# Performance work log

Hardware: AMD Instinct MI355X
Metric: run time of the kernel (lower is better)

The kernel has to match this reference:

```python
import jax, jax.numpy as jnp
import numpy as np


def setup_inputs() -> dict:
    key = jax.random.key(0)
    ks = jax.random.split(key, 7)
    b, c, h, w = 4, 256, 64, 64
    ci = c // 2
    inp = {
        "x0": jax.random.normal(ks[0], (b, 2 * c, h, w), dtype=jnp.float32),
        "x": jax.random.normal(ks[1], (b, c, h, w), dtype=jnp.float32),
        "x_dsm": jax.random.normal(ks[2], (b, c, h, w), dtype=jnp.float32),
        # 1x1 conv weights, stored as [out_ch, in_ch]
        "w_phi": jax.random.normal(ks[3], (ci, c), dtype=jnp.float32) * 0.02,
        "w_theta": jax.random.normal(ks[4], (ci, c), dtype=jnp.float32) * 0.02,
        "w_g": jax.random.normal(ks[5], (c, 2 * c), dtype=jnp.float32) * 0.02,
        "w_mask": jax.random.normal(ks[6], (2 * c, c), dtype=jnp.float32) * 0.02,
    }
    return inp


def reference(x0, x, x_dsm, w_phi, w_theta, w_g, w_mask):
    b, c, h, w = x.shape
    ci = c // 2
    n = h * w
    # 1x1 convs as channel matmuls
    phi = jnp.einsum('oc,bchw->bohw', w_phi, x).reshape(b, ci, n)            # [b, ci, N]
    theta = jnp.einsum('oc,bchw->bohw', w_theta, x_dsm).reshape(b, ci, n)    # [b, ci, N]
    theta = theta.transpose(0, 2, 1)                                         # [b, N, ci]
    g = jnp.einsum('oc,bchw->bohw', w_g, x0).reshape(b, c, n).transpose(0, 2, 1)  # [b, N, c]
    scores = jnp.matmul(theta, phi)                                          # [b, N, N]
    # NOTE: original uses nn.Softmax(dim=1) -> normalize over the FIRST N axis
    attn = jax.nn.softmax(scores, axis=1)
    out = jnp.matmul(attn, g)                                                # [b, N, c]
    out = out.transpose(0, 2, 1).reshape(b, c, h, w)
    mask = jnp.einsum('oc,bchw->bohw', w_mask, out)                          # [b, 2c, h, w]
    return mask + x0
```

## Files before the change

### kernel.cpp

```cpp
#include <hip/hip_runtime.h>
#include <math.h>

#define NB 4
#define NC 256
#define NCI 128
#define NC2 512
#define NPOS 4096
#define ISPLIT 8

using bf16x8 = __attribute__((ext_vector_type(8))) short;
using f32x4  = __attribute__((ext_vector_type(4))) float;

__device__ inline unsigned short f2bf(float f) {
  unsigned int u = __float_as_uint(f);
  u = (u + 0x7fffu + ((u >> 16) & 1u)) >> 16;
  return (unsigned short)u;
}
__device__ inline float bf2f(short s) {
  return __uint_as_float(((unsigned int)(unsigned short)s) << 16);
}

__global__ void k_cast4(const float* __restrict__ s0, short* __restrict__ d0, int n0,
                        const float* __restrict__ s1, short* __restrict__ d1, int n1,
                        const float* __restrict__ s2, short* __restrict__ d2, int n2,
                        const float* __restrict__ s3, short* __restrict__ d3, int n3) {
  int i = blockIdx.x * 256 + threadIdx.x;
  if (i < n0) { d0[i] = (short)f2bf(s0[i]); return; } i -= n0;
  if (i < n1) { d1[i] = (short)f2bf(s1[i]); return; } i -= n1;
  if (i < n2) { d2[i] = (short)f2bf(s2[i]); return; } i -= n2;
  if (i < n3) { d3[i] = (short)f2bf(s3[i]); }
}

__global__ __launch_bounds__(256) void k_tcast_all(
    const float* __restrict__ x, const float* __restrict__ xdsm,
    const float* __restrict__ x0, short* __restrict__ xT,
    short* __restrict__ xdT, short* __restrict__ x0T) {
  __shared__ float t[64][65];
  const int tid = threadIdx.x;
  const int y = blockIdx.y, c0 = blockIdx.x * 64, b = blockIdx.z;
  const float* in; short* out; int R, r0;
  if (y < 4)      { in = x;    out = xT;  R = NC;  r0 = y * 64; }
  else if (y < 8) { in = xdsm; out = xdT; R = NC;  r0 = (y - 4) * 64; }
  else            { in = x0;   out = x0T; R = NC2; r0 = (y - 8) * 64; }
  const size_t inBs = (size_t)R * NPOS, outBs = (size_t)NPOS * R;
  {
    int r = tid >> 2, cc = (tid & 3) * 16;
    const float* ib = in + (size_t)b * inBs + (size_t)(r0 + r) * NPOS + c0 + cc;
#pragma unroll
    for (int i = 0; i < 4; ++i) {
      float4 v = *(const float4*)(ib + i * 4);
      t[r][cc + i * 4 + 0] = v.x; t[r][cc + i * 4 + 1] = v.y;
      t[r][cc + i * 4 + 2] = v.z; t[r][cc + i * 4 + 3] = v.w;
    }
  }
  __syncthreads();
  {
    int c = tid >> 2, rr = (tid & 3) * 16;
    __align__(16) short v[16];
#pragma unroll
    for (int i = 0; i < 16; ++i) v[i] = (short)f2bf(t[rr + i][c]);
    short* ob = out + (size_t)b * outBs + (size_t)(c0 + c) * R + r0 + rr;
    *(int4*)(ob) = *(const int4*)(v);
    *(int4*)(ob + 8) = *(const int4*)(v + 8);
  }
}

__global__ __launch_bounds__(256) void k_tcast4(
    const short* __restrict__ inP, short* __restrict__ out) {
  __shared__ float t[64][65];
  const int tid = threadIdx.x;
  const int r0 = blockIdx.y * 64, c0 = blockIdx.x * 64, b = blockIdx.z;
  {
    int r = tid >> 2, cc = (tid & 3) * 16;
    float tacc[16] = {};
#pragma unroll
    for (int p = 0; p < 4; ++p) {
      const short* ib = inP + ((size_t)p * NB + b) * NC * NPOS +
                        (size_t)(r0 + r) * NPOS + c0 + cc;
      bf16x8 a = *(const bf16x8*)(ib);
      bf16x8 a2 = *(const bf16x8*)(ib + 8);
#pragma unroll
      for (int i = 0; i < 8; ++i) { tacc[i] += bf2f(a[i]); tacc[8 + i] += bf2f(a2[i]); }
    }
#pragma unroll
    for (int i = 0; i < 16; ++i) t[r][cc + i] = tacc[i];
  }
  __syncthreads();
  {
    int c = tid >> 2, rr = (tid & 3) * 16;
    __align__(16) short v[16];
#pragma unroll
    for (int i = 0; i < 16; ++i) v[i] = (short)f2bf(t[rr + i][c]);
    short* ob = out + (size_t)b * (size_t)NPOS * NC + (size_t)(c0 + c) * NC + r0 + rr;
    *(int4*)(ob) = *(const int4*)(v);
    *(int4*)(ob + 8) = *(const int4*)(v + 8);
  }
}

template<bool OUT_BF16, bool HAS_RES>
__global__ __launch_bounds__(256, 2) void k_gemm(
    const short* __restrict__ A, const short* __restrict__ B,
    void* __restrict__ outv, const float* __restrict__ res,
    int K, int sN, size_t aBs, size_t bBs, size_t oBs) {
  __shared__ short As[2][64 * 64];
  __shared__ short Bs_[2][64 * 64];
  const int tid = threadIdx.x, lane = tid & 63, w = tid >> 6;
  const int x = lane & 15, q = lane >> 4;
  const int wm = (w & 1) * 32, wn = (w >> 1) * 32;
  const int n0 = blockIdx.x * 64, m0 = blockIdx.y * 64, b = blockIdx.z;
  const short* Ab = A + (size_t)b * aBs + (size_t)m0 * K;
  const short* Bb = B + (size_t)b * bBs + (size_t)n0 * K;
  const int r = tid >> 2, cth = tid & 3;
  f32x4 acc[2][2];
  acc[0][0] = acc[0][1] = acc[1][0] = acc[1][1] = (f32x4){0.f, 0.f, 0.f, 0.f};
  int4 ra[2], rb[2];
  const int NK = K >> 6;
#define GLOAD(kt)                                                              \
  { _Pragma("unroll") for (int i = 0; i < 2; ++i) {                            \
      ra[i] = *(const int4*)(Ab + (size_t)r * K + (kt) * 64 + (cth + i * 4) * 8); \
      rb[i] = *(const int4*)(Bb + (size_t)r * K + (kt) * 64 + (cth + i * 4) * 8); } }
#define GWRITE(buf)                                                            \
  { _Pragma("unroll") for (int i = 0; i < 2; ++i) {                            \
      *(int4*)(&As[buf][r * 64 + (((cth + i * 4) ^ (r & 7)) * 8)]) = ra[i];    \
      *(int4*)(&Bs_[buf][r * 64 + (((cth + i * 4) ^ (r & 7)) * 8)]) = rb[i]; } }
  GLOAD(0); GWRITE(0); __syncthreads();
  int cur = 0;
  for (int kt = 0; kt < NK; ++kt) {
    if (kt + 1 < NK) GLOAD(kt + 1);
    bf16x8 af[2][2], bfr[2][2];
#pragma unroll
    for (int ms = 0; ms < 2; ++ms) {
      int rowm = wm + ms * 16 + x;
#pragma unroll
      for (int ks = 0; ks < 2; ++ks)
        af[ms][ks] = *(const bf16x8*)(&As[cur][rowm * 64 + (((ks * 4 + q) ^ (rowm & 7)) * 8)]);
    }
#pragma unroll
    for (int ns = 0; ns < 2; ++ns) {
      int rown = wn + ns * 16 + x;
#pragma unroll
      for (int ks = 0; ks < 2; ++ks)
        bfr[ns][ks] = *(const bf16x8*)(&Bs_[cur][rown * 64 + (((ks * 4 + q) ^ (rown & 7)) * 8)]);
    }
#pragma unroll
    for (int ms = 0; ms < 2; ++ms)
#pragma unroll
      for (int ns = 0; ns < 2; ++ns)
#pragma unroll
        for (int ks = 0; ks < 2; ++ks)
          acc[ms][ns] = __builtin_amdgcn_mfma_f32_16x16x32_bf16(
              af[ms][ks], bfr[ns][ks], acc[ms][ns], 0, 0, 0);
    if (kt + 1 < NK) GWRITE(cur ^ 1);
    __syncthreads();
    cur ^= 1;
  }
#pragma unroll
  for (int ms = 0; ms < 2; ++ms)
#pragma unroll
    for (int ns = 0; ns < 2; ++ns) {
      int n = n0 + wn + ns * 16 + x;
      int m = m0 + wm + ms * 16 + q * 4;
      size_t off = (size_t)b * oBs + (size_t)n * sN + m;
      if (OUT_BF16) {
        __align__(8) short pv[4];
#pragma unroll
        for (int j = 0; j < 4; ++j) pv[j] = (short)f2bf(acc[ms][ns][j]);
        *(uint2*)((short*)outv + off) = *(const uint2*)pv;
      } else {
        float4 v = {acc[ms][ns][0], acc[ms][ns][1], acc[ms][ns][2], acc[ms][ns][3]};
        if (HAS_RES) {
          float4 rv = *(const float4*)(res + off);
          v.x += rv.x; v.y += rv.y; v.z += rv.z; v.w += rv.w;
        }
        *(float4*)((float*)outv + off) = v;
      }
    }
#undef GLOAD
#undef GWRITE
}

__global__ __launch_bounds__(256, 4) void k_lsum(
    const short* __restrict__ phiB, const short* __restrict__ thetaB,
    float* __restrict__ plsum) {
  __shared__ short thT[2][64 * 128];
  const int tid = threadIdx.x, lane = tid & 63, w = tid >> 6;
  const int x = lane & 15, q = lane >> 4;
  const int j0 = blockIdx.x * 64, iy = blockIdx.y, b = blockIdx.z;
  const short* phb = phiB + (size_t)b * NPOS * NCI;
  const short* thb = thetaB + (size_t)b * NPOS * NCI + (size_t)iy * (NPOS / ISPLIT) * NCI;
  bf16x8 af[4];
  {
    const short* pr = phb + (size_t)(j0 + w * 16 + x) * NCI;
#pragma unroll
    for (int kk = 0; kk < 4; ++kk) af[kk] = *(const bf16x8*)(pr + kk * 32 + q * 8);
  }
  float lsum[4] = {0.f, 0.f, 0.f, 0.f};
  int4 rt[4];
  const int NIT = NPOS / ISPLIT / 64;
#define LSUM_LOAD(it)                                                         \
  { _Pragma("unroll") for (int r = 0; r < 4; ++r) {                           \
      int s = tid + r * 256; int row = s >> 4, c = s & 15;                    \
      rt[r] = *(const int4*)(thb + (size_t)((it) * 64 + row) * NCI + c * 8); } }
#define LSUM_WRITE(buf)                                                       \
  { _Pragma("unroll") for (int r = 0; r < 4; ++r) {                           \
      int s = tid + r * 256; int row = s >> 4, c = s & 15;                    \
      *(int4*)(&thT[buf][row * 128 + ((c ^ (row & 7)) * 8)]) = rt[r]; } }
  LSUM_LOAD(0); LSUM_WRITE(0); __syncthreads();
  int cur = 0;
  for (int it = 0; it < NIT; ++it) {
    if (it + 1 < NIT) LSUM_LOAD(it + 1);
#pragma unroll
    for (int ii = 0; ii < 4; ++ii) {
      f32x4 s = {0.f, 0.f, 0.f, 0.f};
      int row = ii * 16 + x;
      int sw = row & 7;
#pragma unroll
      for (int kk = 0; kk < 4; ++kk) {
        bf16x8 bfv = *(const bf16x8*)(&thT[cur][row * 128 + (((kk * 4 + q) ^ sw) * 8)]);
        s = __builtin_amdgcn_mfma_f32_16x16x32_bf16(af[kk], bfv, s, 0, 0, 0);
      }
#pragma unroll
      for (int r = 0; r < 4; ++r) lsum[r] += __expf(s[r]);
    }
    if (it + 1 < NIT) LSUM_WRITE(cur ^ 1);
    __syncthreads();
    cur ^= 1;
  }
#pragma unroll
  for (int m = 1; m < 16; m <<= 1)
#pragma unroll
    for (int r = 0; r < 4; ++r) lsum[r] += __shfl_xor(lsum[r], m);
  if (x == 0) {
#pragma unroll
    for (int r = 0; r < 4; ++r)
      plsum[((size_t)(b * ISPLIT + iy) << 12) + j0 + w * 16 + 4 * q + r] = lsum[r];
  }
#undef LSUM_LOAD
#undef LSUM_WRITE
}

__global__ void k_lcomb(const float* __restrict__ plsum, float* __restrict__ linv) {
  int i = blockIdx.x * 256 + threadIdx.x;
  int b = i >> 12, j = i & (NPOS - 1);
  float s = 0.f;
#pragma unroll
  for (int t = 0; t < ISPLIT; ++t) s += plsum[((size_t)(b * ISPLIT + t) << 12) + j];
  linv[i] = 1.0f / s;
}

__global__ void k_scale_g(short* __restrict__ gB, const float* __restrict__ linv) {
  size_t e = ((size_t)blockIdx.x * 256 + threadIdx.x) * 8;
  int b = (int)(e >> 20);
  int p = (int)(e & (NPOS - 1));
  __align__(16) short v[8];
  *(int4*)v = *(const int4*)(gB + e);
  const float* lv = linv + ((size_t)b << 12) + p;
#pragma unroll
  for (int k = 0; k < 8; ++k) v[k] = (short)f2bf(bf2f(v[k]) * lv[k]);
  *(int4*)(gB + e) = *(const int4*)v;
}

__global__ __launch_bounds__(256, 3) void k_attn(
    const short* __restrict__ phiB, const short* __restrict__ thetaB,
    const short* __restrict__ gB, short* __restrict__ omidP) {
  __shared__ short phiT[2][32 * 128];
  __shared__ short gT[2][256 * 32];
  __shared__ short pT[4][16 * 32];
  const int tid = threadIdx.x, lane = tid & 63, w = tid >> 6;
  const int x = lane & 15, q = lane >> 4;
  const int i0 = blockIdx.x * 64, jq = blockIdx.y, b = blockIdx.z;
  const short* phb = phiB + (size_t)b * NPOS * NCI;
  const short* thb = thetaB + (size_t)b * NPOS * NCI;
  const short* gb = gB + (size_t)b * NC * NPOS;
  short* om = omidP + ((size_t)(jq * NB + b)) * NC * NPOS;

  bf16x8 tf[4];
  {
    const short* tr = thb + (size_t)(i0 + w * 16 + x) * NCI;
#pragma unroll
    for (int kk = 0; kk < 4; ++kk) tf[kk] = *(const bf16x8*)(tr + kk * 32 + q * 8);
  }
  f32x4 acc[16];
#pragma unroll
  for (int i = 0; i < 16; ++i) acc[i] = (f32x4){0.f, 0.f, 0.f, 0.f};

  const int sgx = (x & 3) ^ ((x >> 2) & 1);
  int4 rphi[2], rg[4];
  const int NT = 32;
  const int jbase = jq * 32;
#define ATTN_LOAD(jt)                                                          \
  { _Pragma("unroll") for (int r = 0; r < 2; ++r) {                            \
      int s = tid + r * 256; int row = s >> 4, c = s & 15;                     \
      rphi[r] = *(const int4*)(phb + (size_t)((jbase + (jt)) * 32 + row) * NCI + c * 8); } \
    _Pragma("unroll") for (int r = 0; r < 4; ++r) {                            \
      int s = tid + r * 256; int cc = s >> 2, c4 = s & 3;                      \
      rg[r] = *(const int4*)(gb + (size_t)cc * NPOS + (jbase + (jt)) * 32 + c4 * 8); } }
#define ATTN_WRITE(buf)                                                        \
  { _Pragma("unroll") for (int r = 0; r < 2; ++r) {                            \
      int s = tid + r * 256; int row = s >> 4, c = s & 15;                     \
      *(int4*)(&phiT[buf][row * 128 + ((c ^ (row & 7)) * 8)]) = rphi[r]; }     \
    _Pragma("unroll") for (int r = 0; r < 4; ++r) {                            \
      int s = tid + r * 256; int cc = s >> 2, c4 = s & 3;                      \
      int sw = (cc & 3) ^ ((cc >> 2) & 1);                                     \
      *(int4*)(&gT[buf][cc * 32 + ((c4 ^ sw) * 8)]) = rg[r]; } }
  ATTN_LOAD(0); ATTN_WRITE(0); __syncthreads();
  int cur = 0;
  for (int jt = 0; jt < NT; ++jt) {
    if (jt + 1 < NT) ATTN_LOAD(jt + 1);
    {
      const short* PH = &phiT[cur][0];
      const short* GT = &gT[cur][0];
      short* PW = &pT[w][0];
#pragma unroll
      for (int jsub = 0; jsub < 2; ++jsub) {
        f32x4 s = {0.f, 0.f, 0.f, 0.f};
        int row = jsub * 16 + x;
        int sw = row & 7;
#pragma unroll
        for (int kk = 0; kk < 4; ++kk) {
          bf16x8 a = *(const bf16x8*)(PH + row * 128 + (((kk * 4 + q) ^ sw) * 8));
          s = __builtin_amdgcn_mfma_f32_16x16x32_bf16(a, tf[kk], s, 0, 0, 0);
        }
        unsigned short p0 = f2bf(__expf(s[0]));
        unsigned short p1 = f2bf(__expf(s[1]));
        unsigned short p2 = f2bf(__expf(s[2]));
        unsigned short p3 = f2bf(__expf(s[3]));
        unsigned int lo = (unsigned int)p0 | ((unsigned int)p1 << 16);
        unsigned int hi = (unsigned int)p2 | ((unsigned int)p3 << 16);
        int byteoff = (x * 64 + jsub * 32 + q * 8) ^ ((((x >> 1) & 3)) << 4);
        *(uint2*)((char*)PW + byteoff) = make_uint2(lo, hi);
      }
      {
        int c = q ^ ((x >> 1) & 3);
        bf16x8 ap = *(const bf16x8*)((const char*)PW + x * 64 + c * 16);
#pragma unroll
        for (int cf = 0; cf < 16; ++cf) {
          bf16x8 bg = *(const bf16x8*)(GT + (cf * 16 + x) * 32 + ((q ^ sgx) * 8));
          acc[cf] = __builtin_amdgcn_mfma_f32_16x16x32_bf16(ap, bg, acc[cf], 0, 0, 0);
        }
      }
    }
    if (jt + 1 < NT) ATTN_WRITE(cur ^ 1);
    __syncthreads();
    cur ^= 1;
  }
#pragma unroll
  for (int cf = 0; cf < 16; ++cf) {
    __align__(8) short pv[4];
#pragma unroll
    for (int j = 0; j < 4; ++j) pv[j] = (short)f2bf(acc[cf][j]);
    size_t o = (size_t)(cf * 16 + x) * NPOS + i0 + w * 16 + 4 * q;
    *(uint2*)(om + o) = *(const uint2*)pv;
  }
#undef ATTN_LOAD
#undef ATTN_WRITE
}

extern "C" void kernel_launch(void* const* d_in, const int* in_sizes, int n_in,
                              void* d_out, int out_size, void* d_ws, size_t ws_size,
                              hipStream_t stream) {
  (void)in_sizes; (void)n_in; (void)out_size; (void)ws_size;
  const float* x0      = (const float*)d_in[0];
  const float* x       = (const float*)d_in[1];
  const float* x_dsm   = (const float*)d_in[2];
  const float* w_phi   = (const float*)d_in[3];
  const float* w_theta = (const float*)d_in[4];
  const float* w_g     = (const float*)d_in[5];
  const float* w_mask  = (const float*)d_in[6];
  float* outp = (float*)d_out;

  short* sp = (short*)d_ws;
  short* wb_phi   = sp; sp += 32768;
  short* wb_theta = sp; sp += 32768;
  short* wb_g     = sp; sp += 131072;
  short* wb_mask  = sp; sp += 131072;
  short* xT   = sp; sp += (size_t)NB * NPOS * NC;
  short* xdT  = sp; sp += (size_t)NB * NPOS * NC;
  short* x0T  = sp; sp += (size_t)NB * NPOS * NC2;
  short* phiB   = sp; sp += (size_t)NB * NPOS * NCI;
  short* thetaB = sp; sp += (size_t)NB * NPOS * NCI;
  short* gBuf   = sp; sp += (size_t)NB * NC * NPOS;
  float* linv = (float*)sp; sp += 2 * (size_t)NB * NPOS;
  float* plsum = (float*)sp;
  short* omidP = xT;
  short* omidT = phiB;

  k_cast4<<<dim3(1280), 256, 0, stream>>>(w_phi, wb_phi, 32768,
                                          w_theta, wb_theta, 32768,
                                          w_g, wb_g, 131072,
                                          w_mask, wb_mask, 131072);

  k_tcast_all<<<dim3(64, 16, NB), 256, 0, stream>>>(x, x_dsm, x0, xT, xdT, x0T);

  k_gemm<true, false><<<dim3(64, 2, NB), 256, 0, stream>>>(
      wb_phi, xT, phiB, nullptr, NC, NCI, 0, (size_t)NPOS * NC, (size_t)NPOS * NCI);
  k_gemm<true, false><<<dim3(64, 2, NB), 256, 0, stream>>>(
      wb_theta, xdT, thetaB, nullptr, NC, NCI, 0, (size_t)NPOS * NC, (size_t)NPOS * NCI);
  k_gemm<true, false><<<dim3(4, 64, NB), 256, 0, stream>>>(
      x0T, wb_g, gBuf, nullptr, NC2, NPOS, (size_t)NPOS * NC2, 0, (size_t)NC * NPOS);

  k_lsum<<<dim3(NPOS / 64, ISPLIT, NB), 256, 0, stream>>>(phiB, thetaB, plsum);
  k_lcomb<<<dim3(NB * NPOS / 256), 256, 0, stream>>>(plsum, linv);
  k_scale_g<<<dim3(2048), 256, 0, stream>>>(gBuf, linv);

  k_attn<<<dim3(64, 4, NB), 256, 0, stream>>>(phiB, thetaB, gBuf, omidP);

  k_tcast4<<<dim3(64, 4, NB), 256, 0, stream>>>(omidP, omidT);

  k_gemm<false, true><<<dim3(8, 64, NB), 256, 0, stream>>>(
      omidT, wb_mask, outp, x0, NC, NPOS, (size_t)NPOS * NC, 0, (size_t)NC2 * NPOS);
}
```

Before: 251.9 us.

## Switch attention kernel to 32x32x16 MFMA with 128-row query tiles

```diff
diff --git a/kernel.cpp b/kernel.cpp
--- a/kernel.cpp
+++ b/kernel.cpp
@@ -10,6 +10,7 @@
 
 using bf16x8 = __attribute__((ext_vector_type(8))) short;
 using f32x4  = __attribute__((ext_vector_type(4))) float;
+using f32x16 = __attribute__((ext_vector_type(16))) float;
 
 __device__ inline unsigned short f2bf(float f) {
   unsigned int u = __float_as_uint(f);
@@ -260,31 +261,33 @@
   *(int4*)(gB + e) = *(const int4*)v;
 }
 
-__global__ __launch_bounds__(256, 3) void k_attn(
+__global__ __launch_bounds__(256, 2) void k_attn(
     const short* __restrict__ phiB, const short* __restrict__ thetaB,
     const short* __restrict__ gB, short* __restrict__ omidP) {
   __shared__ short phiT[2][32 * 128];
   __shared__ short gT[2][256 * 32];
-  __shared__ short pT[4][16 * 32];
+  __shared__ short pT[4][32 * 32];
   const int tid = threadIdx.x, lane = tid & 63, w = tid >> 6;
-  const int x = lane & 15, q = lane >> 4;
-  const int i0 = blockIdx.x * 64, jq = blockIdx.y, b = blockIdx.z;
+  const int il = lane & 31, h = lane >> 5;
+  const int key = (il >> 1) & 3;
+  const int i0 = blockIdx.x * 128, jq = blockIdx.y, b = blockIdx.z;
   const short* phb = phiB + (size_t)b * NPOS * NCI;
   const short* thb = thetaB + (size_t)b * NPOS * NCI;
   const short* gb = gB + (size_t)b * NC * NPOS;
   short* om = omidP + ((size_t)(jq * NB + b)) * NC * NPOS;
 
-  bf16x8 tf[4];
-  {
-    const short* tr = thb + (size_t)(i0 + w * 16 + x) * NCI;
-#pragma unroll
-    for (int kk = 0; kk < 4; ++kk) tf[kk] = *(const bf16x8*)(tr + kk * 32 + q * 8);
-  }
-  f32x4 acc[16];
-#pragma unroll
-  for (int i = 0; i < 16; ++i) acc[i] = (f32x4){0.f, 0.f, 0.f, 0.f};
-
-  const int sgx = (x & 3) ^ ((x >> 2) & 1);
+  bf16x8 tf[8];
+  {
+    const short* tr = thb + (size_t)(i0 + w * 32 + il) * NCI;
+#pragma unroll
+    for (int kk = 0; kk < 8; ++kk) tf[kk] = *(const bf16x8*)(tr + kk * 16 + h * 8);
+  }
+  f32x16 acc[8];
+#pragma unroll
+  for (int i = 0; i < 8; ++i)
+#pragma unroll
+    for (int r = 0; r < 16; ++r) acc[i][r] = 0.f;
+
   int4 rphi[2], rg[4];
   const int NT = 32;
   const int jbase = jq * 32;
@@ -301,42 +304,44 @@
       *(int4*)(&phiT[buf][row * 128 + ((c ^ (row & 7)) * 8)]) = rphi[r]; }     \
     _Pragma("unroll") for (int r = 0; r < 4; ++r) {                            \
       int s = tid + r * 256; int cc = s >> 2, c4 = s & 3;                      \
-      int sw = (cc & 3) ^ ((cc >> 2) & 1);                                     \
-      *(int4*)(&gT[buf][cc * 32 + ((c4 ^ sw) * 8)]) = rg[r]; } }
+      *(int4*)(&gT[buf][cc * 32 + ((c4 ^ ((cc >> 1) & 3)) * 8)]) = rg[r]; } }
   ATTN_LOAD(0); ATTN_WRITE(0); __syncthreads();
   int cur = 0;
   for (int jt = 0; jt < NT; ++jt) {
     if (jt + 1 < NT) ATTN_LOAD(jt + 1);
     {
       const short* PH = &phiT[cur][0];
+      short* PW = &pT[w][0];
+      f32x16 s16;
+#pragma unroll
+      for (int r = 0; r < 16; ++r) s16[r] = 0.f;
+      const int swp = il & 7;
+#pragma unroll
+      for (int kk = 0; kk < 8; ++kk) {
+        bf16x8 a = *(const bf16x8*)(PH + il * 128 + (((2 * kk + h) ^ swp) * 8));
+        s16 = __builtin_amdgcn_mfma_f32_32x32x16_bf16(a, tf[kk], s16, 0, 0, 0);
+      }
+#pragma unroll
+      for (int g2 = 0; g2 < 4; ++g2) {
+        unsigned short p0 = f2bf(__expf(s16[4 * g2 + 0]));
+        unsigned short p1 = f2bf(__expf(s16[4 * g2 + 1]));
+        unsigned short p2 = f2bf(__expf(s16[4 * g2 + 2]));
+        unsigned short p3 = f2bf(__expf(s16[4 * g2 + 3]));
+        unsigned int lo = (unsigned int)p0 | ((unsigned int)p1 << 16);
+        unsigned int hi2 = (unsigned int)p2 | ((unsigned int)p3 << 16);
+        *(uint2*)(PW + il * 32 + ((g2 ^ key) * 8) + 4 * h) = make_uint2(lo, hi2);
+      }
       const short* GT = &gT[cur][0];
-      short* PW = &pT[w][0];
-#pragma unroll
-      for (int jsub = 0; jsub < 2; ++jsub) {
-        f32x4 s = {0.f, 0.f, 0.f, 0.f};
-        int row = jsub * 16 + x;
-        int sw = row & 7;
-#pragma unroll
-        for (int kk = 0; kk < 4; ++kk) {
-          bf16x8 a = *(const bf16x8*)(PH + row * 128 + (((kk * 4 + q) ^ sw) * 8));
-          s = __builtin_amdgcn_mfma_f32_16x16x32_bf16(a, tf[kk], s, 0, 0, 0);
-        }
-        unsigned short p0 = f2bf(__expf(s[0]));
-        unsigned short p1 = f2bf(__expf(s[1]));
-        unsigned short p2 = f2bf(__expf(s[2]));
-        unsigned short p3 = f2bf(__expf(s[3]));
-        unsigned int lo = (unsigned int)p0 | ((unsigned int)p1 << 16);
-        unsigned int hi = (unsigned int)p2 | ((unsigned int)p3 << 16);
-        int byteoff = (x * 64 + jsub * 32 + q * 8) ^ ((((x >> 1) & 3)) << 4);
-        *(uint2*)((char*)PW + byteoff) = make_uint2(lo, hi);
-      }
-      {
-        int c = q ^ ((x >> 1) & 3);
-        bf16x8 ap = *(const bf16x8*)((const char*)PW + x * 64 + c * 16);
-#pragma unroll
-        for (int cf = 0; cf < 16; ++cf) {
-          bf16x8 bg = *(const bf16x8*)(GT + (cf * 16 + x) * 32 + ((q ^ sgx) * 8));
-          acc[cf] = __builtin_amdgcn_mfma_f32_16x16x32_bf16(ap, bg, acc[cf], 0, 0, 0);
+      bf16x8 pa[2];
+#pragma unroll
+      for (int jh2 = 0; jh2 < 2; ++jh2)
+        pa[jh2] = *(const bf16x8*)(PW + il * 32 + (((2 * jh2 + h) ^ key) * 8));
+#pragma unroll
+      for (int ct = 0; ct < 8; ++ct) {
+#pragma unroll
+        for (int jh2 = 0; jh2 < 2; ++jh2) {
+          bf16x8 bg = *(const bf16x8*)(GT + (ct * 32 + il) * 32 + (((2 * jh2 + h) ^ key) * 8));
+          acc[ct] = __builtin_amdgcn_mfma_f32_32x32x16_bf16(pa[jh2], bg, acc[ct], 0, 0, 0);
         }
       }
     }
@@ -345,13 +350,15 @@
     cur ^= 1;
   }
 #pragma unroll
-  for (int cf = 0; cf < 16; ++cf) {
-    __align__(8) short pv[4];
-#pragma unroll
-    for (int j = 0; j < 4; ++j) pv[j] = (short)f2bf(acc[cf][j]);
-    size_t o = (size_t)(cf * 16 + x) * NPOS + i0 + w * 16 + 4 * q;
-    *(uint2*)(om + o) = *(const uint2*)pv;
-  }
+  for (int ct = 0; ct < 8; ++ct)
+#pragma unroll
+    for (int g2 = 0; g2 < 4; ++g2) {
+      __align__(8) short pv[4];
+#pragma unroll
+      for (int e = 0; e < 4; ++e) pv[e] = (short)f2bf(acc[ct][4 * g2 + e]);
+      size_t o = (size_t)(ct * 32 + il) * NPOS + i0 + w * 32 + 8 * g2 + 4 * h;
+      *(uint2*)(om + o) = *(const uint2*)pv;
+    }
 #undef ATTN_LOAD
 #undef ATTN_WRITE
 }
@@ -403,7 +410,7 @@
   k_lcomb<<<dim3(NB * NPOS / 256), 256, 0, stream>>>(plsum, linv);
   k_scale_g<<<dim3(2048), 256, 0, stream>>>(gBuf, linv);
 
-  k_attn<<<dim3(64, 4, NB), 256, 0, stream>>>(phiB, thetaB, gBuf, omidP);
+  k_attn<<<dim3(NPOS / 128, 4, NB), 256, 0, stream>>>(phiB, thetaB, gBuf, omidP);
 
   k_tcast4<<<dim3(64, 4, NB), 256, 0, stream>>>(omidP, omidT);
 
```

Result: faster. 236.9 us (-6.0%).
